# Performance work log

Hardware: AMD Instinct MI355X
Metric: run time of the kernel (lower is better)

Reference implementation:

```python
import jax, jax.numpy as jnp
import numpy as np

D_MODEL = 256
N_HEADS = 8
S_LOCAL = (3, 3)
EPS = 1e-6
B, T, H, W = 2, 4, 32, 32


def _neighbor_idx(Hs, Ws, kh, kw):
    # Replicates nn.Unfold(kernel=(kh,kw), padding=(kh//2,kw//2), stride=1) ordering:
    # kernel offsets row-major, spatial positions row-major.
    off_i = np.repeat(np.arange(kh) - kh // 2, kw)  # (L,)
    off_j = np.tile(np.arange(kw) - kw // 2, kh)    # (L,)
    pi, pj = np.meshgrid(np.arange(Hs), np.arange(Ws), indexing='ij')
    ni = pi.reshape(-1, 1) + off_i[None, :]  # (N, L)
    nj = pj.reshape(-1, 1) + off_j[None, :]
    valid = (ni >= 0) & (ni < Hs) & (nj >= 0) & (nj < Ws)
    idx = np.clip(ni, 0, Hs - 1) * Ws + np.clip(nj, 0, Ws - 1)
    return jnp.asarray(idx, dtype=jnp.int32), jnp.asarray(valid)


def setup_inputs() -> dict:
    key = jax.random.key(0)
    ks = jax.random.split(key, 10)
    D = D_MODEL
    x = jax.random.normal(ks[0], (B, D, T, H, W), dtype=jnp.float32)
    w = lambda k: jax.random.normal(k, (D, D), dtype=jnp.float32) * 0.02
    return {
        'x': x,
        'gamma': jnp.ones((D,), jnp.float32),
        'beta': jnp.zeros((D,), jnp.float32),
        'Wq': w(ks[1]), 'Wk': w(ks[2]), 'Wv': w(ks[3]),
        'Wkl': w(ks[4]), 'Wvl': w(ks[5]), 'Wo': w(ks[6]),
        'q_bias': jax.random.normal(ks[7], (1, N_HEADS, 1, D // N_HEADS), dtype=jnp.float32) * 0.02,
    }


def reference(x, gamma, beta, Wq, Wk, Wv, Wkl, Wvl, Wo, q_bias):
    Bx, D, Tx, Hx, Wx = x.shape
    N = Hx * Wx
    BT = Bx * Tx
    h = N_HEADS
    dh = D // h
    factor = dh ** -0.5

    # (B, D, T, H, W) -> (B*T, H*W, D)
    xr = x.transpose(0, 2, 3, 4, 1).reshape(BT, N, D)
    mu = xr.mean(-1, keepdims=True)
    var = ((xr - mu) ** 2).mean(-1, keepdims=True)
    xn = (xr - mu) * jax.lax.rsqrt(var + EPS) * gamma + beta

    def proj(Wm):
        return (xn @ Wm.T).reshape(BT, N, h, dh).transpose(0, 2, 1, 3)  # (BT, h, N, dh)

    q = proj(Wq) + q_bias
    k = proj(Wk)
    v = proj(Wv)
    kl = proj(Wkl)
    vl = proj(Wvl)

    idx, valid = _neighbor_idx(Hx, Wx, *S_LOCAL)  # (N, L)
    k_nb = kl[:, :, idx, :]  # (BT, h, N, L, dh) -- gather instead of im2col
    v_nb = vl[:, :, idx, :]

    attn_global = jnp.einsum('bhnd,bhgd->bhng', q, k) * factor         # (BT,h,N,N)
    attn_local = jnp.einsum('bhnd,bhnld->bhnl', q, k_nb)               # (BT,h,N,L)
    attn_local = jnp.where(valid[None, None], attn_local, -jnp.inf) * factor

    attn = jax.nn.softmax(jnp.concatenate([attn_global, attn_local], axis=-1), axis=-1)
    a_g, a_l = attn[..., :N], attn[..., N:]

    xg = jnp.einsum('bhng,bhgd->bhnd', a_g, v)
    xl = jnp.einsum('bhnl,bhnld->bhnd', a_l, v_nb)
    out = ((xg + xl).transpose(0, 2, 1, 3).reshape(BT, N, D)) @ Wo.T
    return out.reshape(Bx, Tx, Hx, Wx, D).transpose(0, 4, 1, 2, 3)
```

## Files before the change

kernel.cpp:

```cpp
#include <hip/hip_runtime.h>

#define NROWS 8192
#define MCONST 8.0f

typedef float f32x4 __attribute__((ext_vector_type(4)));
typedef __bf16 bf16x8 __attribute__((ext_vector_type(8)));
typedef __bf16 bf16x4 __attribute__((ext_vector_type(4)));

__global__ __launch_bounds__(256) void ln_kernel(const float* __restrict__ x,
                                                 const float* __restrict__ gamma,
                                                 const float* __restrict__ beta,
                                                 __bf16* __restrict__ xnh,
                                                 __bf16* __restrict__ xnl) {
  __shared__ float red[2][8][32];
  const int blk = blockIdx.x;
  const int bt = blk >> 5;
  const int b = bt >> 2, t = bt & 3;
  const int n0 = (blk & 31) << 5;
  const int part = threadIdx.x >> 5, r = threadIdx.x & 31;
  const int n = n0 + r;
  const float* xp = x + ((size_t)(b * 256) * 4 + t) * 1024 + n;
  float sum = 0.f, sumsq = 0.f;
#pragma unroll 8
  for (int dd = 0; dd < 32; ++dd) {
    float vv = xp[(size_t)(part * 32 + dd) * 4096];
    sum += vv;
    sumsq += vv * vv;
  }
  red[0][part][r] = sum;
  red[1][part][r] = sumsq;
  __syncthreads();
  float s1 = 0.f, s2 = 0.f;
#pragma unroll
  for (int p = 0; p < 8; ++p) {
    s1 += red[0][p][r];
    s2 += red[1][p][r];
  }
  const float mu = s1 * (1.0f / 256.0f);
  const float var = s2 * (1.0f / 256.0f) - mu * mu;
  const float rstd = rsqrtf(var + 1e-6f);
  const size_t row = (size_t)bt * 1024 + n;
  __bf16 hbuf[32], lbuf[32];
#pragma unroll 8
  for (int dd = 0; dd < 32; ++dd) {
    const int d = part * 32 + dd;
    float vv = xp[(size_t)d * 4096];
    const float val = (vv - mu) * rstd * gamma[d] + beta[d];
    const __bf16 h = (__bf16)val;
    hbuf[dd] = h;
    lbuf[dd] = (__bf16)(val - (float)h);
  }
  __bf16* oh = xnh + row * 256 + part * 32;
  __bf16* ol = xnl + row * 256 + part * 32;
#pragma unroll
  for (int f = 0; f < 4; ++f) {
    *(bf16x8*)(oh + f * 8) = *(bf16x8*)&hbuf[f * 8];
    *(bf16x8*)(ol + f * 8) = *(bf16x8*)&lbuf[f * 8];
  }
}

__global__ __launch_bounds__(256) void wsplit_kernel(
    const float* __restrict__ Wq, const float* __restrict__ Wk,
    const float* __restrict__ Wv, const float* __restrict__ Wkl,
    const float* __restrict__ Wvl, const float* __restrict__ Wo,
    __bf16* __restrict__ wh, __bf16* __restrict__ wl) {
  const int gid = blockIdx.x * 256 + threadIdx.x;
  const int mat = gid >> 14;
  const int off = (gid & 16383) * 4;
  const float* W = (mat == 0) ? Wq : (mat == 1) ? Wk : (mat == 2) ? Wv
                   : (mat == 3) ? Wkl : (mat == 4) ? Wvl : Wo;
  const float4 f = *(const float4*)(W + off);
  bf16x4 h, l;
  h[0] = (__bf16)f.x; l[0] = (__bf16)(f.x - (float)h[0]);
  h[1] = (__bf16)f.y; l[1] = (__bf16)(f.y - (float)h[1]);
  h[2] = (__bf16)f.z; l[2] = (__bf16)(f.z - (float)h[2]);
  h[3] = (__bf16)f.w; l[3] = (__bf16)(f.w - (float)h[3]);
  *(bf16x4*)(wh + (size_t)mat * 65536 + off) = h;
  *(bf16x4*)(wl + (size_t)mat * 65536 + off) = l;
}

#define ASTR 40
__global__ __launch_bounds__(256) void proj_kernel(
    const __bf16* __restrict__ xnh, const __bf16* __restrict__ xnl,
    const __bf16* __restrict__ wh, const __bf16* __restrict__ wl,
    const float* __restrict__ qb,
    __bf16* __restrict__ qh_g, __bf16* __restrict__ ql_g,
    __bf16* __restrict__ khF, __bf16* __restrict__ klF,
    __bf16* __restrict__ vfH, __bf16* __restrict__ vfL,
    float* __restrict__ kloc, float* __restrict__ vloc) {
  __shared__ __bf16 Ah[128 * ASTR], Al[128 * ASTR];
  __shared__ __bf16 Bh[128 * ASTR], Bl[128 * ASTR];
  const int z = blockIdx.z;
  const __bf16* Wh = wh + (size_t)z * 65536;
  const __bf16* Wl = wl + (size_t)z * 65536;
  const int m0 = blockIdx.x * 128;
  const int o0 = blockIdx.y * 128;
  const int tid = threadIdx.x;
  const int w = tid >> 6, lane = tid & 63;
  const int col = lane & 15, grp = lane >> 4;
  const int mq = (w & 1) * 64, nq = (w >> 1) * 64;
  f32x4 acc[4][4];
#pragma unroll
  for (int i = 0; i < 4; ++i)
#pragma unroll
    for (int j = 0; j < 4; ++j) acc[i][j] = (f32x4){0.f, 0.f, 0.f, 0.f};

#pragma unroll 1
  for (int k0 = 0; k0 < 256; k0 += 32) {
    const int sg = tid & 3, rowq = tid >> 2;
#pragma unroll
    for (int p = 0; p < 2; ++p) {
      const int m = p * 64 + rowq;
      const size_t srcA = (size_t)(m0 + m) * 256 + k0 + sg * 8;
      *(bf16x8*)&Ah[m * ASTR + sg * 8] = *(const bf16x8*)(xnh + srcA);
      *(bf16x8*)&Al[m * ASTR + sg * 8] = *(const bf16x8*)(xnl + srcA);
      const size_t srcB = (size_t)(o0 + m) * 256 + k0 + sg * 8;
      *(bf16x8*)&Bh[m * ASTR + sg * 8] = *(const bf16x8*)(Wh + srcB);
      *(bf16x8*)&Bl[m * ASTR + sg * 8] = *(const bf16x8*)(Wl + srcB);
    }
    __syncthreads();
    bf16x8 ah[4], al[4], bh[4], bl[4];
#pragma unroll
    for (int mi = 0; mi < 4; ++mi) {
      ah[mi] = *(const bf16x8*)&Ah[(mq + mi * 16 + col) * ASTR + 8 * grp];
      al[mi] = *(const bf16x8*)&Al[(mq + mi * 16 + col) * ASTR + 8 * grp];
    }
#pragma unroll
    for (int ni = 0; ni < 4; ++ni) {
      bh[ni] = *(const bf16x8*)&Bh[(nq + ni * 16 + col) * ASTR + 8 * grp];
      bl[ni] = *(const bf16x8*)&Bl[(nq + ni * 16 + col) * ASTR + 8 * grp];
    }
#pragma unroll
    for (int mi = 0; mi < 4; ++mi)
#pragma unroll
      for (int ni = 0; ni < 4; ++ni) {
        acc[mi][ni] = __builtin_amdgcn_mfma_f32_16x16x32_bf16(al[mi], bh[ni], acc[mi][ni], 0, 0, 0);
        acc[mi][ni] = __builtin_amdgcn_mfma_f32_16x16x32_bf16(ah[mi], bl[ni], acc[mi][ni], 0, 0, 0);
        acc[mi][ni] = __builtin_amdgcn_mfma_f32_16x16x32_bf16(ah[mi], bh[ni], acc[mi][ni], 0, 0, 0);
      }
    __syncthreads();
  }
#pragma unroll
  for (int mi = 0; mi < 4; ++mi) {
    const int mb = m0 + mq + mi * 16 + grp * 4;
    const int bt = mb >> 10;
    const int nb = mb & 1023;
#pragma unroll
    for (int ni = 0; ni < 4; ++ni) {
      const int o = o0 + nq + ni * 16 + col;
      const int head = o >> 5, dh = o & 31;
      const int bth = bt * 8 + head;
      if (z == 2) {
        const int ch = nb >> 6, s = (nb >> 5) & 1, h2 = dh >> 4;
        const int vgrp = (nb >> 3) & 3, j0 = nb & 7;
        const int vlane = vgrp * 16 + (dh & 15);
        const size_t off = (((size_t)(bth * 16 + ch) * 4) + h2 * 2 + s) * 512 + vlane * 8 + j0;
        bf16x4 hv, lv;
#pragma unroll
        for (int r = 0; r < 4; ++r) {
          const float val = acc[mi][ni][r];
          const __bf16 h = (__bf16)val;
          hv[r] = h;
          lv[r] = (__bf16)(val - (float)h);
        }
        *(bf16x4*)(vfH + off) = hv;
        *(bf16x4*)(vfL + off) = lv;
      } else if (z <= 1) {
        const float qbo = (z == 0) ? qb[o] : 0.f;
#pragma unroll
        for (int r = 0; r < 4; ++r) {
          const float val = acc[mi][ni][r] + qbo;
          const __bf16 h = (__bf16)val;
          if (z == 0) {
            const size_t idx = ((size_t)bth * 1024 + nb + r) * 32 + dh;
            qh_g[idx] = h;
            ql_g[idx] = (__bf16)(val - (float)h);
          } else {
            const int key = nb + r;
            const int tile = key >> 4, kcol = key & 15;
            const int kgrp = dh >> 3, j = dh & 7;
            const size_t off = ((size_t)(bth * 64 + tile)) * 512 + (kgrp * 16 + kcol) * 8 + j;
            khF[off] = h;
            klF[off] = (__bf16)(val - (float)h);
          }
        }
      } else {
        float* dst = (z == 3) ? kloc : vloc;
#pragma unroll
        for (int r = 0; r < 4; ++r)
          dst[((size_t)bth * 1024 + nb + r) * 32 + dh] = acc[mi][ni][r];
      }
    }
  }
}

#define PSTR 68
__global__ __launch_bounds__(256) void attn_kernel(
    const __bf16* __restrict__ qh_g, const __bf16* __restrict__ ql_g,
    const __bf16* __restrict__ khF, const __bf16* __restrict__ klF,
    const __bf16* __restrict__ vfH, const __bf16* __restrict__ vfL,
    const float* __restrict__ kloc, const float* __restrict__ vloc,
    __bf16* __restrict__ ctxh, __bf16* __restrict__ ctxl) {
  __shared__ float pbs[4][16 * PSTR];
  float* obuf = &pbs[0][0];

  const int bth = blockIdx.x, qt = blockIdx.y;
  const int tid = threadIdx.x;
  const int w = tid >> 6, lane = tid & 63;
  const int col = lane & 15, grp = lane >> 4;
  const int m0 = qt * 64 + w * 16;
  const float SCALE2 = 0.17677669529663687f * 1.4426950408889634f;
  const size_t kvbase = (size_t)bth << 10;
  float* pb = pbs[w];

  const __bf16* khB = khF + (size_t)bth * 32768 + lane * 8;
  const __bf16* klB = klF + (size_t)bth * 32768 + lane * 8;
  const __bf16* vhB = vfH + (size_t)bth * 32768 + lane * 8;
  const __bf16* vlB = vfL + (size_t)bth * 32768 + lane * 8;

  const bf16x8 qhf = *(const bf16x8*)(qh_g + (kvbase + m0 + col) * 32 + 8 * grp);
  const bf16x8 qlf = *(const bf16x8*)(ql_g + (kvbase + m0 + col) * 32 + 8 * grp);

  f32x4 oc0 = {0.f, 0.f, 0.f, 0.f}, oc1 = {0.f, 0.f, 0.f, 0.f};
  float lrow[4] = {0.f, 0.f, 0.f, 0.f};

  bf16x8 kh4[4], kl4[4];
  bf16x8 vh[2][2], vl[2][2];

#pragma unroll
  for (int t = 0; t < 4; ++t) {
    kh4[t] = *(const bf16x8*)(khB + (size_t)t * 512);
    kl4[t] = *(const bf16x8*)(klB + (size_t)t * 512);
  }
  {
    f32x4 s_[4];
#pragma unroll
    for (int t = 0; t < 4; ++t) {
      f32x4 a2 = {0.f, 0.f, 0.f, 0.f};
      a2 = __builtin_amdgcn_mfma_f32_16x16x32_bf16(qlf, kh4[t], a2, 0, 0, 0);
      a2 = __builtin_amdgcn_mfma_f32_16x16x32_bf16(qhf, kl4[t], a2, 0, 0, 0);
      a2 = __builtin_amdgcn_mfma_f32_16x16x32_bf16(qhf, kh4[t], a2, 0, 0, 0);
      s_[t] = a2;
    }
#pragma unroll
    for (int r = 0; r < 4; ++r)
#pragma unroll
      for (int t = 0; t < 4; ++t) {
        const float p = __builtin_amdgcn_exp2f(fmaf(s_[t][r], SCALE2, -MCONST));
        lrow[r] += p;
        pb[(grp * 4 + r) * PSTR + t * 16 + col] = p;
      }
  }

#pragma unroll 1
  for (int i = 1; i < 16; ++i) {
#pragma unroll
    for (int h = 0; h < 2; ++h)
#pragma unroll
      for (int s = 0; s < 2; ++s) {
        const size_t off = ((size_t)(i - 1) * 4 + h * 2 + s) * 512;
        vh[h][s] = *(const bf16x8*)(vhB + off);
        vl[h][s] = *(const bf16x8*)(vlB + off);
      }
#pragma unroll
    for (int t = 0; t < 4; ++t) {
      kh4[t] = *(const bf16x8*)(khB + ((size_t)i * 4 + t) * 512);
      kl4[t] = *(const bf16x8*)(klB + ((size_t)i * 4 + t) * 512);
    }
    f32x4 pa[4];
#pragma unroll
    for (int s = 0; s < 2; ++s) {
      pa[s * 2 + 0] = *(const f32x4*)&pb[col * PSTR + s * 32 + 8 * grp];
      pa[s * 2 + 1] = *(const f32x4*)&pb[col * PSTR + s * 32 + 8 * grp + 4];
    }
    bf16x8 ph[2], pl[2];
#pragma unroll
    for (int s = 0; s < 2; ++s)
#pragma unroll
      for (int j = 0; j < 4; ++j) {
        const __bf16 h0 = (__bf16)pa[s * 2][j];
        ph[s][j] = h0;
        pl[s][j] = (__bf16)(pa[s * 2][j] - (float)h0);
        const __bf16 h1 = (__bf16)pa[s * 2 + 1][j];
        ph[s][4 + j] = h1;
        pl[s][4 + j] = (__bf16)(pa[s * 2 + 1][j] - (float)h1);
      }
#pragma unroll
    for (int s = 0; s < 2; ++s) {
      oc0 = __builtin_amdgcn_mfma_f32_16x16x32_bf16(pl[s], vh[0][s], oc0, 0, 0, 0);
      oc0 = __builtin_amdgcn_mfma_f32_16x16x32_bf16(ph[s], vl[0][s], oc0, 0, 0, 0);
      oc0 = __builtin_amdgcn_mfma_f32_16x16x32_bf16(ph[s], vh[0][s], oc0, 0, 0, 0);
      oc1 = __builtin_amdgcn_mfma_f32_16x16x32_bf16(pl[s], vh[1][s], oc1, 0, 0, 0);
      oc1 = __builtin_amdgcn_mfma_f32_16x16x32_bf16(ph[s], vl[1][s], oc1, 0, 0, 0);
      oc1 = __builtin_amdgcn_mfma_f32_16x16x32_bf16(ph[s], vh[1][s], oc1, 0, 0, 0);
    }
    f32x4 s_[4];
#pragma unroll
    for (int t = 0; t < 4; ++t) {
      f32x4 a2 = {0.f, 0.f, 0.f, 0.f};
      a2 = __builtin_amdgcn_mfma_f32_16x16x32_bf16(qlf, kh4[t], a2, 0, 0, 0);
      a2 = __builtin_amdgcn_mfma_f32_16x16x32_bf16(qhf, kl4[t], a2, 0, 0, 0);
      a2 = __builtin_amdgcn_mfma_f32_16x16x32_bf16(qhf, kh4[t], a2, 0, 0, 0);
      s_[t] = a2;
    }
#pragma unroll
    for (int r = 0; r < 4; ++r)
#pragma unroll
      for (int t = 0; t < 4; ++t) {
        const float p = __builtin_amdgcn_exp2f(fmaf(s_[t][r], SCALE2, -MCONST));
        lrow[r] += p;
        pb[(grp * 4 + r) * PSTR + t * 16 + col] = p;
      }
  }

  {
#pragma unroll
    for (int h = 0; h < 2; ++h)
#pragma unroll
      for (int s = 0; s < 2; ++s) {
        const size_t off = ((size_t)15 * 4 + h * 2 + s) * 512;
        vh[h][s] = *(const bf16x8*)(vhB + off);
        vl[h][s] = *(const bf16x8*)(vlB + off);
      }
    f32x4 pa[4];
#pragma unroll
    for (int s = 0; s < 2; ++s) {
      pa[s * 2 + 0] = *(const f32x4*)&pb[col * PSTR + s * 32 + 8 * grp];
      pa[s * 2 + 1] = *(const f32x4*)&pb[col * PSTR + s * 32 + 8 * grp + 4];
    }
    bf16x8 ph[2], pl[2];
#pragma unroll
    for (int s = 0; s < 2; ++s)
#pragma unroll
      for (int j = 0; j < 4; ++j) {
        const __bf16 h0 = (__bf16)pa[s * 2][j];
        ph[s][j] = h0;
        pl[s][j] = (__bf16)(pa[s * 2][j] - (float)h0);
        const __bf16 h1 = (__bf16)pa[s * 2 + 1][j];
        ph[s][4 + j] = h1;
        pl[s][4 + j] = (__bf16)(pa[s * 2 + 1][j] - (float)h1);
      }
#pragma unroll
    for (int s = 0; s < 2; ++s) {
      oc0 = __builtin_amdgcn_mfma_f32_16x16x32_bf16(pl[s], vh[0][s], oc0, 0, 0, 0);
      oc0 = __builtin_amdgcn_mfma_f32_16x16x32_bf16(ph[s], vl[0][s], oc0, 0, 0, 0);
      oc0 = __builtin_amdgcn_mfma_f32_16x16x32_bf16(ph[s], vh[0][s], oc0, 0, 0, 0);
      oc1 = __builtin_amdgcn_mfma_f32_16x16x32_bf16(pl[s], vh[1][s], oc1, 0, 0, 0);
      oc1 = __builtin_amdgcn_mfma_f32_16x16x32_bf16(ph[s], vl[1][s], oc1, 0, 0, 0);
      oc1 = __builtin_amdgcn_mfma_f32_16x16x32_bf16(ph[s], vh[1][s], oc1, 0, 0, 0);
    }
  }

#pragma unroll
  for (int r = 0; r < 4; ++r) {
    lrow[r] += __shfl_xor(lrow[r], 1);
    lrow[r] += __shfl_xor(lrow[r], 2);
    lrow[r] += __shfl_xor(lrow[r], 4);
    lrow[r] += __shfl_xor(lrow[r], 8);
  }

  __syncthreads();
#pragma unroll
  for (int r = 0; r < 4; ++r) {
    const int qq = w * 16 + grp * 4 + r;
    obuf[qq * 36 + col] = oc0[r];
    obuf[qq * 36 + 16 + col] = oc1[r];
    if (col == 0) obuf[qq * 36 + 33] = lrow[r];
  }
  __syncthreads();

  {
    const int qq = tid >> 2, part = tid & 3;
    const int n = qt * 64 + qq;
    float L = obuf[qq * 36 + 33];
    float A[8];
#pragma unroll
    for (int d = 0; d < 8; ++d) A[d] = obuf[qq * 36 + part * 8 + d];
    float qrf[8];
    {
      const bf16x8 qh8 = *(const bf16x8*)(qh_g + (kvbase + n) * 32 + part * 8);
      const bf16x8 ql8 = *(const bf16x8*)(ql_g + (kvbase + n) * 32 + part * 8);
#pragma unroll
      for (int d = 0; d < 8; ++d)
        qrf[d] = ((float)qh8[d] + (float)ql8[d]) * SCALE2;
    }
    const int pi = n >> 5, pj = n & 31;
#pragma unroll
    for (int tt = 0; tt < 9; ++tt) {
      const int ni = pi + tt / 3 - 1;
      const int nj = pj + tt % 3 - 1;
      const bool ok = (ni >= 0) && (ni < 32) && (nj >= 0) && (nj < 32);
      if (ok) {
        const size_t nb = (kvbase + ni * 32 + nj) * 32 + part * 8;
        const float* kr = kloc + nb;
        float d0 = 0.f, d1 = 0.f;
#pragma unroll
        for (int d = 0; d < 8; d += 2) {
          d0 = fmaf(qrf[d], kr[d], d0);
          d1 = fmaf(qrf[d + 1], kr[d + 1], d1);
        }
        float dot = d0 + d1;
        dot += __shfl_xor(dot, 1);
        dot += __shfl_xor(dot, 2);
        const float p = __builtin_amdgcn_exp2f(dot - MCONST);
        L += p;
        const float* vr = vloc + nb;
#pragma unroll
        for (int d = 0; d < 8; ++d) A[d] = fmaf(p, vr[d], A[d]);
      }
    }
    const float inv = 1.0f / L;
    const int bt = bth >> 3, head = bth & 7;
    __bf16 hb[8], lb[8];
#pragma unroll
    for (int d = 0; d < 8; ++d) {
      const float val = A[d] * inv;
      const __bf16 h = (__bf16)val;
      hb[d] = h;
      lb[d] = (__bf16)(val - (float)h);
    }
    const size_t cb = ((size_t)(bt * 1024 + n)) * 256 + head * 32 + part * 8;
    *(bf16x8*)(ctxh + cb) = *(bf16x8*)hb;
    *(bf16x8*)(ctxl + cb) = *(bf16x8*)lb;
  }
}

__global__ __launch_bounds__(256) void outproj_kernel(
    const __bf16* __restrict__ ctxh, const __bf16* __restrict__ ctxl,
    const __bf16* __restrict__ woh, const __bf16* __restrict__ wol,
    float* __restrict__ out) {
  __shared__ __bf16 Ah[128 * ASTR], Al[128 * ASTR];
  __shared__ __bf16 Bh[128 * ASTR], Bl[128 * ASTR];
  const int m0 = blockIdx.x * 128;
  const int o0 = blockIdx.y * 128;
  const int tid = threadIdx.x;
  const int w = tid >> 6, lane = tid & 63;
  const int col = lane & 15, grp = lane >> 4;
  const int mq = (w & 1) * 64, nq = (w >> 1) * 64;
  f32x4 acc[4][4];
#pragma unroll
  for (int i = 0; i < 4; ++i)
#pragma unroll
    for (int j = 0; j < 4; ++j) acc[i][j] = (f32x4){0.f, 0.f, 0.f, 0.f};

#pragma unroll 1
  for (int k0 = 0; k0 < 256; k0 += 32) {
    const int sg = tid & 3, rowq = tid >> 2;
#pragma unroll
    for (int p = 0; p < 2; ++p) {
      const int m = p * 64 + rowq;
      const size_t srcA = (size_t)(m0 + m) * 256 + k0 + sg * 8;
      *(bf16x8*)&Ah[m * ASTR + sg * 8] = *(const bf16x8*)(ctxh + srcA);
      *(bf16x8*)&Al[m * ASTR + sg * 8] = *(const bf16x8*)(ctxl + srcA);
      const size_t srcB = (size_t)(o0 + m) * 256 + k0 + sg * 8;
      *(bf16x8*)&Bh[m * ASTR + sg * 8] = *(const bf16x8*)(woh + srcB);
      *(bf16x8*)&Bl[m * ASTR + sg * 8] = *(const bf16x8*)(wol + srcB);
    }
    __syncthreads();
    bf16x8 ah[4], al[4], bh[4], bl[4];
#pragma unroll
    for (int mi = 0; mi < 4; ++mi) {
      ah[mi] = *(const bf16x8*)&Ah[(mq + mi * 16 + col) * ASTR + 8 * grp];
      al[mi] = *(const bf16x8*)&Al[(mq + mi * 16 + col) * ASTR + 8 * grp];
    }
#pragma unroll
    for (int ni = 0; ni < 4; ++ni) {
      bh[ni] = *(const bf16x8*)&Bh[(nq + ni * 16 + col) * ASTR + 8 * grp];
      bl[ni] = *(const bf16x8*)&Bl[(nq + ni * 16 + col) * ASTR + 8 * grp];
    }
#pragma unroll
    for (int mi = 0; mi < 4; ++mi)
#pragma unroll
      for (int ni = 0; ni < 4; ++ni) {
        acc[mi][ni] = __builtin_amdgcn_mfma_f32_16x16x32_bf16(al[mi], bh[ni], acc[mi][ni], 0, 0, 0);
        acc[mi][ni] = __builtin_amdgcn_mfma_f32_16x16x32_bf16(ah[mi], bl[ni], acc[mi][ni], 0, 0, 0);
        acc[mi][ni] = __builtin_amdgcn_mfma_f32_16x16x32_bf16(ah[mi], bh[ni], acc[mi][ni], 0, 0, 0);
      }
    __syncthreads();
  }
#pragma unroll
  for (int mi = 0; mi < 4; ++mi) {
    const int mb = m0 + mq + mi * 16 + grp * 4;
    const int bt = mb >> 10;
    const int nb = mb & 1023;
    const int b = bt >> 2, t = bt & 3;
#pragma unroll
    for (int ni = 0; ni < 4; ++ni) {
      const int o = o0 + nq + ni * 16 + col;
      const float4 f4 = make_float4(acc[mi][ni][0], acc[mi][ni][1],
                                    acc[mi][ni][2], acc[mi][ni][3]);
      *(float4*)&out[((size_t)(b * 256 + o) * 4 + t) * 1024 + nb] = f4;
    }
  }
}

extern "C" void kernel_launch(void* const* d_in, const int* in_sizes, int n_in,
                              void* d_out, int out_size, void* d_ws, size_t ws_size,
                              hipStream_t stream) {
  const float* x = (const float*)d_in[0];
  const float* gamma = (const float*)d_in[1];
  const float* beta = (const float*)d_in[2];
  const float* Wq = (const float*)d_in[3];
  const float* Wk = (const float*)d_in[4];
  const float* Wv = (const float*)d_in[5];
  const float* Wkl = (const float*)d_in[6];
  const float* Wvl = (const float*)d_in[7];
  const float* Wo = (const float*)d_in[8];
  const float* qb = (const float*)d_in[9];

  char* base = (char*)d_ws;
  const size_t MB = 1024 * 1024;
  __bf16* xnh = (__bf16*)(base + 0);
  __bf16* xnl = (__bf16*)(base + 4 * MB);
  __bf16* ctxh = (__bf16*)(base + 0);
  __bf16* ctxl = (__bf16*)(base + 4 * MB);
  __bf16* wh = (__bf16*)(base + 8 * MB);
  __bf16* wl = (__bf16*)(base + 8 * MB + 768 * 1024);
  __bf16* qh = (__bf16*)(base + 10 * MB);
  __bf16* ql = (__bf16*)(base + 14 * MB);
  __bf16* khF = (__bf16*)(base + 18 * MB);
  __bf16* klF = (__bf16*)(base + 22 * MB);
  __bf16* vfH = (__bf16*)(base + 26 * MB);
  __bf16* vfL = (__bf16*)(base + 30 * MB);
  float* kloc = (float*)(base + 34 * MB);
  float* vloc = (float*)(base + 42 * MB);

  hipLaunchKernelGGL(ln_kernel, dim3(256), dim3(256), 0, stream, x, gamma, beta,
                     xnh, xnl);
  hipLaunchKernelGGL(wsplit_kernel, dim3(384), dim3(256), 0, stream, Wq, Wk, Wv,
                     Wkl, Wvl, Wo, wh, wl);
  hipLaunchKernelGGL(proj_kernel, dim3(64, 2, 5), dim3(256), 0, stream, xnh, xnl,
                     wh, wl, qb, qh, ql, khF, klF, vfH, vfL, kloc, vloc);
  hipLaunchKernelGGL(attn_kernel, dim3(64, 16), dim3(256), 0, stream, qh, ql, khF,
                     klF, vfH, vfL, kloc, vloc, ctxh, ctxl);
  hipLaunchKernelGGL(outproj_kernel, dim3(64, 2), dim3(256), 0, stream, ctxh, ctxl,
                     wh + (size_t)5 * 65536, wl + (size_t)5 * 65536, (float*)d_out);
}
```

Before: 181.4 us.

## Store activations and weights in MFMA fragment layout and drop LDS staging in GEMMs

LayerNorm, weight split and attention output now write their bf16 hi/lo data directly in a 16x32 MFMA fragment-tiled layout. The projection and output-projection GEMMs can then load operands straight from global memory into registers, removing shared-memory staging and the barriers around it. For the non-V projections the operand roles are swapped so results come out as 4 consecutive head dims, which allows vectorized bf16x4/float4 stores. The trade-off is that there is no LDS reuse of tiles across waves, so operands are re-read from global/L2 by each wave.

```diff
diff --git a/kernel.cpp b/kernel.cpp
--- a/kernel.cpp
+++ b/kernel.cpp
@@ -1,17 +1,17 @@
 #include <hip/hip_runtime.h>
 
-#define NROWS 8192
 #define MCONST 8.0f
 
 typedef float f32x4 __attribute__((ext_vector_type(4)));
 typedef __bf16 bf16x8 __attribute__((ext_vector_type(8)));
 typedef __bf16 bf16x4 __attribute__((ext_vector_type(4)));
 
+
 __global__ __launch_bounds__(256) void ln_kernel(const float* __restrict__ x,
                                                  const float* __restrict__ gamma,
                                                  const float* __restrict__ beta,
-                                                 __bf16* __restrict__ xnh,
-                                                 __bf16* __restrict__ xnl) {
+                                                 __bf16* __restrict__ xfh,
+                                                 __bf16* __restrict__ xfl) {
   __shared__ float red[2][8][32];
   const int blk = blockIdx.x;
   const int bt = blk >> 5;
@@ -50,12 +50,11 @@
     hbuf[dd] = h;
     lbuf[dd] = (__bf16)(val - (float)h);
   }
-  __bf16* oh = xnh + row * 256 + part * 32;
-  __bf16* ol = xnl + row * 256 + part * 32;
-#pragma unroll
-  for (int f = 0; f < 4; ++f) {
-    *(bf16x8*)(oh + f * 8) = *(bf16x8*)&hbuf[f * 8];
-    *(bf16x8*)(ol + f * 8) = *(bf16x8*)&lbuf[f * 8];
+  const size_t base = ((row >> 4) * 8 + part) * 512 + (row & 15) * 8;
+#pragma unroll
+  for (int g = 0; g < 4; ++g) {
+    *(bf16x8*)(xfh + base + g * 128) = *(bf16x8*)&hbuf[g * 8];
+    *(bf16x8*)(xfl + base + g * 128) = *(bf16x8*)&lbuf[g * 8];
   }
 }
 
@@ -66,39 +65,43 @@
     __bf16* __restrict__ wh, __bf16* __restrict__ wl) {
   const int gid = blockIdx.x * 256 + threadIdx.x;
   const int mat = gid >> 14;
-  const int off = (gid & 16383) * 4;
+  const int e = (gid & 16383) * 4;
   const float* W = (mat == 0) ? Wq : (mat == 1) ? Wk : (mat == 2) ? Wv
                    : (mat == 3) ? Wkl : (mat == 4) ? Wvl : Wo;
-  const float4 f = *(const float4*)(W + off);
+  const float4 f = *(const float4*)(W + e);
+  const int o = e >> 8, k = e & 255;
+  const size_t frag = (size_t)mat * 65536 + ((o >> 4) * 8 + (k >> 5)) * 512 +
+                      (((k & 31) >> 3) * 16 + (o & 15)) * 8 + (k & 7);
   bf16x4 h, l;
   h[0] = (__bf16)f.x; l[0] = (__bf16)(f.x - (float)h[0]);
   h[1] = (__bf16)f.y; l[1] = (__bf16)(f.y - (float)h[1]);
   h[2] = (__bf16)f.z; l[2] = (__bf16)(f.z - (float)h[2]);
   h[3] = (__bf16)f.w; l[3] = (__bf16)(f.w - (float)h[3]);
-  *(bf16x4*)(wh + (size_t)mat * 65536 + off) = h;
-  *(bf16x4*)(wl + (size_t)mat * 65536 + off) = l;
+  *(bf16x4*)(wh + frag) = h;
+  *(bf16x4*)(wl + frag) = l;
 }
 
-#define ASTR 40
 __global__ __launch_bounds__(256) void proj_kernel(
-    const __bf16* __restrict__ xnh, const __bf16* __restrict__ xnl,
+    const __bf16* __restrict__ xfh, const __bf16* __restrict__ xfl,
     const __bf16* __restrict__ wh, const __bf16* __restrict__ wl,
     const float* __restrict__ qb,
     __bf16* __restrict__ qh_g, __bf16* __restrict__ ql_g,
     __bf16* __restrict__ khF, __bf16* __restrict__ klF,
     __bf16* __restrict__ vfH, __bf16* __restrict__ vfL,
     float* __restrict__ kloc, float* __restrict__ vloc) {
-  __shared__ __bf16 Ah[128 * ASTR], Al[128 * ASTR];
-  __shared__ __bf16 Bh[128 * ASTR], Bl[128 * ASTR];
   const int z = blockIdx.z;
-  const __bf16* Wh = wh + (size_t)z * 65536;
-  const __bf16* Wl = wl + (size_t)z * 65536;
-  const int m0 = blockIdx.x * 128;
+  const int tok0 = blockIdx.x * 128;
   const int o0 = blockIdx.y * 128;
   const int tid = threadIdx.x;
   const int w = tid >> 6, lane = tid & 63;
   const int col = lane & 15, grp = lane >> 4;
-  const int mq = (w & 1) * 64, nq = (w >> 1) * 64;
+  const int oq = (w & 1) * 64, tq = (w >> 1) * 64;
+
+  const __bf16* wbh = wh + (size_t)z * 65536 + (size_t)((o0 + oq) >> 4) * 8 * 512 + lane * 8;
+  const __bf16* wbl = wl + (size_t)z * 65536 + (size_t)((o0 + oq) >> 4) * 8 * 512 + lane * 8;
+  const __bf16* xbh = xfh + (size_t)((tok0 + tq) >> 4) * 8 * 512 + lane * 8;
+  const __bf16* xbl = xfl + (size_t)((tok0 + tq) >> 4) * 8 * 512 + lane * 8;
+
   f32x4 acc[4][4];
 #pragma unroll
   for (int i = 0; i < 4; ++i)
@@ -106,89 +109,96 @@
     for (int j = 0; j < 4; ++j) acc[i][j] = (f32x4){0.f, 0.f, 0.f, 0.f};
 
 #pragma unroll 1
-  for (int k0 = 0; k0 < 256; k0 += 32) {
-    const int sg = tid & 3, rowq = tid >> 2;
-#pragma unroll
-    for (int p = 0; p < 2; ++p) {
-      const int m = p * 64 + rowq;
-      const size_t srcA = (size_t)(m0 + m) * 256 + k0 + sg * 8;
-      *(bf16x8*)&Ah[m * ASTR + sg * 8] = *(const bf16x8*)(xnh + srcA);
-      *(bf16x8*)&Al[m * ASTR + sg * 8] = *(const bf16x8*)(xnl + srcA);
-      const size_t srcB = (size_t)(o0 + m) * 256 + k0 + sg * 8;
-      *(bf16x8*)&Bh[m * ASTR + sg * 8] = *(const bf16x8*)(Wh + srcB);
-      *(bf16x8*)&Bl[m * ASTR + sg * 8] = *(const bf16x8*)(Wl + srcB);
-    }
-    __syncthreads();
-    bf16x8 ah[4], al[4], bh[4], bl[4];
-#pragma unroll
-    for (int mi = 0; mi < 4; ++mi) {
-      ah[mi] = *(const bf16x8*)&Ah[(mq + mi * 16 + col) * ASTR + 8 * grp];
-      al[mi] = *(const bf16x8*)&Al[(mq + mi * 16 + col) * ASTR + 8 * grp];
-    }
-#pragma unroll
-    for (int ni = 0; ni < 4; ++ni) {
-      bh[ni] = *(const bf16x8*)&Bh[(nq + ni * 16 + col) * ASTR + 8 * grp];
-      bl[ni] = *(const bf16x8*)&Bl[(nq + ni * 16 + col) * ASTR + 8 * grp];
-    }
-#pragma unroll
-    for (int mi = 0; mi < 4; ++mi)
-#pragma unroll
-      for (int ni = 0; ni < 4; ++ni) {
-        acc[mi][ni] = __builtin_amdgcn_mfma_f32_16x16x32_bf16(al[mi], bh[ni], acc[mi][ni], 0, 0, 0);
-        acc[mi][ni] = __builtin_amdgcn_mfma_f32_16x16x32_bf16(ah[mi], bl[ni], acc[mi][ni], 0, 0, 0);
-        acc[mi][ni] = __builtin_amdgcn_mfma_f32_16x16x32_bf16(ah[mi], bh[ni], acc[mi][ni], 0, 0, 0);
-      }
-    __syncthreads();
-  }
-#pragma unroll
-  for (int mi = 0; mi < 4; ++mi) {
-    const int mb = m0 + mq + mi * 16 + grp * 4;
-    const int bt = mb >> 10;
-    const int nb = mb & 1023;
-#pragma unroll
-    for (int ni = 0; ni < 4; ++ni) {
-      const int o = o0 + nq + ni * 16 + col;
-      const int head = o >> 5, dh = o & 31;
-      const int bth = bt * 8 + head;
-      if (z == 2) {
-        const int ch = nb >> 6, s = (nb >> 5) & 1, h2 = dh >> 4;
-        const int vgrp = (nb >> 3) & 3, j0 = nb & 7;
-        const int vlane = vgrp * 16 + (dh & 15);
-        const size_t off = (((size_t)(bth * 16 + ch) * 4) + h2 * 2 + s) * 512 + vlane * 8 + j0;
+  for (int kc = 0; kc < 8; ++kc) {
+    bf16x8 wfh_[4], wfl_[4], xh_[4], xl_[4];
+#pragma unroll
+    for (int i = 0; i < 4; ++i) {
+      wfh_[i] = *(const bf16x8*)(wbh + ((size_t)i * 8 + kc) * 512);
+      wfl_[i] = *(const bf16x8*)(wbl + ((size_t)i * 8 + kc) * 512);
+      xh_[i] = *(const bf16x8*)(xbh + ((size_t)i * 8 + kc) * 512);
+      xl_[i] = *(const bf16x8*)(xbl + ((size_t)i * 8 + kc) * 512);
+    }
+    if (z == 2) {
+#pragma unroll
+      for (int i = 0; i < 4; ++i)
+#pragma unroll
+        for (int j = 0; j < 4; ++j) {
+          acc[i][j] = __builtin_amdgcn_mfma_f32_16x16x32_bf16(xl_[i], wfh_[j], acc[i][j], 0, 0, 0);
+          acc[i][j] = __builtin_amdgcn_mfma_f32_16x16x32_bf16(xh_[i], wfl_[j], acc[i][j], 0, 0, 0);
+          acc[i][j] = __builtin_amdgcn_mfma_f32_16x16x32_bf16(xh_[i], wfh_[j], acc[i][j], 0, 0, 0);
+        }
+    } else {
+#pragma unroll
+      for (int i = 0; i < 4; ++i)
+#pragma unroll
+        for (int j = 0; j < 4; ++j) {
+          acc[i][j] = __builtin_amdgcn_mfma_f32_16x16x32_bf16(wfl_[i], xh_[j], acc[i][j], 0, 0, 0);
+          acc[i][j] = __builtin_amdgcn_mfma_f32_16x16x32_bf16(wfh_[i], xl_[j], acc[i][j], 0, 0, 0);
+          acc[i][j] = __builtin_amdgcn_mfma_f32_16x16x32_bf16(wfh_[i], xh_[j], acc[i][j], 0, 0, 0);
+        }
+    }
+  }
+
+  if (z == 2) {
+#pragma unroll
+    for (int i = 0; i < 4; ++i) {
+      const int tk = tok0 + tq + i * 16 + grp * 4;
+      const int bt = tk >> 10, nb = tk & 1023;
+      const int ch = nb >> 6, ss = (nb >> 5) & 1;
+      const int vgrp = (nb >> 3) & 3, j0 = nb & 7;
+#pragma unroll
+      for (int j = 0; j < 4; ++j) {
+        const int o = o0 + oq + j * 16 + col;
+        const int head = o >> 5, dh = o & 31;
+        const int bth = bt * 8 + head;
+        const size_t off = (((size_t)(bth * 16 + ch) * 4) + (dh >> 4) * 2 + ss) * 512 +
+                           (vgrp * 16 + (dh & 15)) * 8 + j0;
         bf16x4 hv, lv;
 #pragma unroll
-        for (int r = 0; r < 4; ++r) {
-          const float val = acc[mi][ni][r];
+        for (int rr = 0; rr < 4; ++rr) {
+          const float val = acc[i][j][rr];
           const __bf16 h = (__bf16)val;
-          hv[r] = h;
-          lv[r] = (__bf16)(val - (float)h);
+          hv[rr] = h;
+          lv[rr] = (__bf16)(val - (float)h);
         }
         *(bf16x4*)(vfH + off) = hv;
         *(bf16x4*)(vfL + off) = lv;
-      } else if (z <= 1) {
-        const float qbo = (z == 0) ? qb[o] : 0.f;
-#pragma unroll
-        for (int r = 0; r < 4; ++r) {
-          const float val = acc[mi][ni][r] + qbo;
-          const __bf16 h = (__bf16)val;
+      }
+    }
+  } else {
+#pragma unroll
+    for (int i = 0; i < 4; ++i) {
+      const int o_ = o0 + oq + i * 16 + grp * 4;
+      const int head = o_ >> 5, dh0 = o_ & 31;
+      float4 qb4 = make_float4(0.f, 0.f, 0.f, 0.f);
+      if (z == 0) qb4 = *(const float4*)&qb[o_];
+#pragma unroll
+      for (int j = 0; j < 4; ++j) {
+        const int n_ = tok0 + tq + j * 16 + col;
+        const int bt = n_ >> 10, nb = n_ & 1023;
+        const int bth = bt * 8 + head;
+        float v0 = acc[i][j][0], v1 = acc[i][j][1], v2 = acc[i][j][2], v3 = acc[i][j][3];
+        if (z == 0) { v0 += qb4.x; v1 += qb4.y; v2 += qb4.z; v3 += qb4.w; }
+        if (z <= 1) {
+          bf16x4 hv, lv;
+          hv[0] = (__bf16)v0; lv[0] = (__bf16)(v0 - (float)hv[0]);
+          hv[1] = (__bf16)v1; lv[1] = (__bf16)(v1 - (float)hv[1]);
+          hv[2] = (__bf16)v2; lv[2] = (__bf16)(v2 - (float)hv[2]);
+          hv[3] = (__bf16)v3; lv[3] = (__bf16)(v3 - (float)hv[3]);
           if (z == 0) {
-            const size_t idx = ((size_t)bth * 1024 + nb + r) * 32 + dh;
-            qh_g[idx] = h;
-            ql_g[idx] = (__bf16)(val - (float)h);
+            const size_t idx = ((size_t)bth * 1024 + nb) * 32 + dh0;
+            *(bf16x4*)(qh_g + idx) = hv;
+            *(bf16x4*)(ql_g + idx) = lv;
           } else {
-            const int key = nb + r;
-            const int tile = key >> 4, kcol = key & 15;
-            const int kgrp = dh >> 3, j = dh & 7;
-            const size_t off = ((size_t)(bth * 64 + tile)) * 512 + (kgrp * 16 + kcol) * 8 + j;
-            khF[off] = h;
-            klF[off] = (__bf16)(val - (float)h);
+            const size_t ka = ((size_t)(bth * 64 + (nb >> 4))) * 512 +
+                              ((dh0 >> 3) * 16 + (nb & 15)) * 8 + (dh0 & 7);
+            *(bf16x4*)(khF + ka) = hv;
+            *(bf16x4*)(klF + ka) = lv;
           }
+        } else {
+          float* dst = (z == 3) ? kloc : vloc;
+          *(float4*)&dst[((size_t)bth * 1024 + nb) * 32 + dh0] = make_float4(v0, v1, v2, v3);
         }
-      } else {
-        float* dst = (z == 3) ? kloc : vloc;
-#pragma unroll
-        for (int r = 0; r < 4; ++r)
-          dst[((size_t)bth * 1024 + nb + r) * 32 + dh] = acc[mi][ni][r];
       }
     }
   }
@@ -200,7 +210,7 @@
     const __bf16* __restrict__ khF, const __bf16* __restrict__ klF,
     const __bf16* __restrict__ vfH, const __bf16* __restrict__ vfL,
     const float* __restrict__ kloc, const float* __restrict__ vloc,
-    __bf16* __restrict__ ctxh, __bf16* __restrict__ ctxl) {
+    __bf16* __restrict__ ctxFh, __bf16* __restrict__ ctxFl) {
   __shared__ float pbs[4][16 * PSTR];
   float* obuf = &pbs[0][0];
 
@@ -419,24 +429,29 @@
       hb[d] = h;
       lb[d] = (__bf16)(val - (float)h);
     }
-    const size_t cb = ((size_t)(bt * 1024 + n)) * 256 + head * 32 + part * 8;
-    *(bf16x8*)(ctxh + cb) = *(bf16x8*)hb;
-    *(bf16x8*)(ctxl + cb) = *(bf16x8*)lb;
+    const size_t rowg = (size_t)bt * 1024 + n;
+    const size_t cb = ((rowg >> 4) * 8 + head) * 512 + (part * 16 + (rowg & 15)) * 8;
+    *(bf16x8*)(ctxFh + cb) = *(bf16x8*)hb;
+    *(bf16x8*)(ctxFl + cb) = *(bf16x8*)lb;
   }
 }
 
 __global__ __launch_bounds__(256) void outproj_kernel(
-    const __bf16* __restrict__ ctxh, const __bf16* __restrict__ ctxl,
+    const __bf16* __restrict__ ctxFh, const __bf16* __restrict__ ctxFl,
     const __bf16* __restrict__ woh, const __bf16* __restrict__ wol,
     float* __restrict__ out) {
-  __shared__ __bf16 Ah[128 * ASTR], Al[128 * ASTR];
-  __shared__ __bf16 Bh[128 * ASTR], Bl[128 * ASTR];
   const int m0 = blockIdx.x * 128;
   const int o0 = blockIdx.y * 128;
   const int tid = threadIdx.x;
   const int w = tid >> 6, lane = tid & 63;
   const int col = lane & 15, grp = lane >> 4;
   const int mq = (w & 1) * 64, nq = (w >> 1) * 64;
+
+  const __bf16* abh = ctxFh + (size_t)((m0 + mq) >> 4) * 8 * 512 + lane * 8;
+  const __bf16* abl = ctxFl + (size_t)((m0 + mq) >> 4) * 8 * 512 + lane * 8;
+  const __bf16* bbh = woh + (size_t)((o0 + nq) >> 4) * 8 * 512 + lane * 8;
+  const __bf16* bbl = wol + (size_t)((o0 + nq) >> 4) * 8 * 512 + lane * 8;
+
   f32x4 acc[4][4];
 #pragma unroll
   for (int i = 0; i < 4; ++i)
@@ -444,29 +459,14 @@
     for (int j = 0; j < 4; ++j) acc[i][j] = (f32x4){0.f, 0.f, 0.f, 0.f};
 
 #pragma unroll 1
-  for (int k0 = 0; k0 < 256; k0 += 32) {
-    const int sg = tid & 3, rowq = tid >> 2;
-#pragma unroll
-    for (int p = 0; p < 2; ++p) {
-      const int m = p * 64 + rowq;
-      const size_t srcA = (size_t)(m0 + m) * 256 + k0 + sg * 8;
-      *(bf16x8*)&Ah[m * ASTR + sg * 8] = *(const bf16x8*)(ctxh + srcA);
-      *(bf16x8*)&Al[m * ASTR + sg * 8] = *(const bf16x8*)(ctxl + srcA);
-      const size_t srcB = (size_t)(o0 + m) * 256 + k0 + sg * 8;
-      *(bf16x8*)&Bh[m * ASTR + sg * 8] = *(const bf16x8*)(woh + srcB);
-      *(bf16x8*)&Bl[m * ASTR + sg * 8] = *(const bf16x8*)(wol + srcB);
-    }
-    __syncthreads();
+  for (int kc = 0; kc < 8; ++kc) {
     bf16x8 ah[4], al[4], bh[4], bl[4];
 #pragma unroll
-    for (int mi = 0; mi < 4; ++mi) {
-      ah[mi] = *(const bf16x8*)&Ah[(mq + mi * 16 + col) * ASTR + 8 * grp];
-      al[mi] = *(const bf16x8*)&Al[(mq + mi * 16 + col) * ASTR + 8 * grp];
-    }
-#pragma unroll
-    for (int ni = 0; ni < 4; ++ni) {
-      bh[ni] = *(const bf16x8*)&Bh[(nq + ni * 16 + col) * ASTR + 8 * grp];
-      bl[ni] = *(const bf16x8*)&Bl[(nq + ni * 16 + col) * ASTR + 8 * grp];
+    for (int i = 0; i < 4; ++i) {
+      ah[i] = *(const bf16x8*)(abh + ((size_t)i * 8 + kc) * 512);
+      al[i] = *(const bf16x8*)(abl + ((size_t)i * 8 + kc) * 512);
+      bh[i] = *(const bf16x8*)(bbh + ((size_t)i * 8 + kc) * 512);
+      bl[i] = *(const bf16x8*)(bbl + ((size_t)i * 8 + kc) * 512);
     }
 #pragma unroll
     for (int mi = 0; mi < 4; ++mi)
@@ -476,7 +476,6 @@
         acc[mi][ni] = __builtin_amdgcn_mfma_f32_16x16x32_bf16(ah[mi], bl[ni], acc[mi][ni], 0, 0, 0);
         acc[mi][ni] = __builtin_amdgcn_mfma_f32_16x16x32_bf16(ah[mi], bh[ni], acc[mi][ni], 0, 0, 0);
       }
-    __syncthreads();
   }
 #pragma unroll
   for (int mi = 0; mi < 4; ++mi) {
@@ -510,10 +509,10 @@
 
   char* base = (char*)d_ws;
   const size_t MB = 1024 * 1024;
-  __bf16* xnh = (__bf16*)(base + 0);
-  __bf16* xnl = (__bf16*)(base + 4 * MB);
-  __bf16* ctxh = (__bf16*)(base + 0);
-  __bf16* ctxl = (__bf16*)(base + 4 * MB);
+  __bf16* xfh = (__bf16*)(base + 0);
+  __bf16* xfl = (__bf16*)(base + 4 * MB);
+  __bf16* ctxFh = (__bf16*)(base + 0);
+  __bf16* ctxFl = (__bf16*)(base + 4 * MB);
   __bf16* wh = (__bf16*)(base + 8 * MB);
   __bf16* wl = (__bf16*)(base + 8 * MB + 768 * 1024);
   __bf16* qh = (__bf16*)(base + 10 * MB);
@@ -526,13 +525,14 @@
   float* vloc = (float*)(base + 42 * MB);
 
   hipLaunchKernelGGL(ln_kernel, dim3(256), dim3(256), 0, stream, x, gamma, beta,
-                     xnh, xnl);
+                     xfh, xfl);
   hipLaunchKernelGGL(wsplit_kernel, dim3(384), dim3(256), 0, stream, Wq, Wk, Wv,
                      Wkl, Wvl, Wo, wh, wl);
-  hipLaunchKernelGGL(proj_kernel, dim3(64, 2, 5), dim3(256), 0, stream, xnh, xnl,
+  hipLaunchKernelGGL(proj_kernel, dim3(64, 2, 5), dim3(256), 0, stream, xfh, xfl,
                      wh, wl, qb, qh, ql, khF, klF, vfH, vfL, kloc, vloc);
   hipLaunchKernelGGL(attn_kernel, dim3(64, 16), dim3(256), 0, stream, qh, ql, khF,
-                     klF, vfH, vfL, kloc, vloc, ctxh, ctxl);
-  hipLaunchKernelGGL(outproj_kernel, dim3(64, 2), dim3(256), 0, stream, ctxh, ctxl,
-                     wh + (size_t)5 * 65536, wl + (size_t)5 * 65536, (float*)d_out);
+                     klF, vfH, vfL, kloc, vloc, ctxFh, ctxFl);
+  hipLaunchKernelGGL(outproj_kernel, dim3(64, 2), dim3(256), 0, stream, ctxFh,
+                     ctxFl, wh + (size_t)5 * 65536, wl + (size_t)5 * 65536,
+                     (float*)d_out);
 }
```

After: 180.6 us. Within noise of the previous version (-0.4%).
